# Kernel tuning notes

Measured on AMD Instinct MI355X. Metric: run time of the kernel, lower is better.

Reference implementation:

```python
import jax, jax.numpy as jnp
import numpy as np

B, L, DIM = 4, 2048, 512
H, D = 8, 64
SCALE = D ** -0.5
NEG = -10000.0


def setup_inputs() -> dict:
    key = jax.random.key(0)
    ks = jax.random.split(key, 5)
    std = 1.0 / np.sqrt(DIM)
    return {
        "x": jax.random.normal(ks[0], (B, L, DIM), dtype=jnp.float32),
        "wq": jax.random.normal(ks[1], (H * D, DIM), dtype=jnp.float32) * std,
        "wk": jax.random.normal(ks[2], (H * D, DIM), dtype=jnp.float32) * std,
        "wv": jax.random.normal(ks[3], (H * D, DIM), dtype=jnp.float32) * std,
        "wo": jax.random.normal(ks[4], (DIM, H * D), dtype=jnp.float32) * std,
    }


def reference(x, wq, wk, wv, wo):
    b, l, _ = x.shape
    # projections (torch Linear: y = x @ W.T), split heads -> [b,h,l,d]
    q = (x @ wq.T).reshape(b, l, H, D).transpose(0, 2, 1, 3)
    k = (x @ wk.T).reshape(b, l, H, D).transpose(0, 2, 1, 3)
    v = (x @ wv.T).reshape(b, l, H, D).transpose(0, 2, 1, 3)
    scores = jnp.einsum("bhld,bhsd->bhls", q, k) * SCALE
    scores = jnp.nan_to_num(scores, nan=0.0, posinf=10000.0, neginf=NEG)
    diag = jnp.eye(l, dtype=bool)[None, None]  # [1,1,l,l]
    scores = jnp.where(diag, NEG, scores)
    attn = jax.nn.softmax(scores, axis=-1)
    attn = jnp.where(diag, 0.0, attn)
    attn = jnp.nan_to_num(attn, nan=0.0, posinf=0.0, neginf=0.0)
    out = jnp.einsum("bhls,bhsd->bhld", attn, v)
    out = out.transpose(0, 2, 1, 3).reshape(b, l, H * D)
    return out @ wo.T
```

## Files before the change

### kernel.cpp

```cpp
#include <hip/hip_runtime.h>
#include <hip/hip_bf16.h>


#define Bsz 4
#define Lsz 2048
#define DIMsz 512
#define Hsz 8
#define Dsz 64

typedef _Float16 f16;
typedef __attribute__((ext_vector_type(8))) _Float16 f16x8;
typedef __attribute__((ext_vector_type(4))) _Float16 f16x4;
typedef __attribute__((ext_vector_type(4))) float f32x4;
typedef unsigned int u32;

#if __has_builtin(__builtin_amdgcn_exp2f)
#define EXP2(x) __builtin_amdgcn_exp2f(x)
#else
#define EXP2(x) __expf(0.6931471805599453f * (x))
#endif

__device__ __forceinline__ void gl2lds16(const void* g, void* l) {
    __builtin_amdgcn_global_load_lds(
        (const __attribute__((address_space(1))) u32*)g,
        (__attribute__((address_space(3))) u32*)l, 16, 0, 0);
}

__global__ __launch_bounds__(256) void pack_f16(
    const float* __restrict__ x, const float* __restrict__ wq,
    const float* __restrict__ wk, const float* __restrict__ wv,
    const float* __restrict__ wo,
    f16* __restrict__ xh, f16* __restrict__ w3h, f16* __restrict__ woh)
{
    const int seg = blockIdx.y;
    const float* s; f16* d; int n; float sc = 1.0f;
    switch (seg) {
        case 0: s = x;  d = xh;            n = 4194304; break;
        case 1: s = wq; d = w3h;           n = 262144; sc = 0.18033688011112042f; break;
        case 2: s = wk; d = w3h + 262144;  n = 262144; break;
        case 3: s = wv; d = w3h + 524288;  n = 262144; break;
        default: s = wo; d = woh;          n = 262144; break;
    }
    int i = (blockIdx.x * 256 + threadIdx.x) * 4;
    if (i >= n) return;
    float4 v = *(const float4*)(s + i);
    f16x4 o;
    o.x = (f16)(v.x * sc); o.y = (f16)(v.y * sc);
    o.z = (f16)(v.z * sc); o.w = (f16)(v.w * sc);
    *(f16x4*)(d + i) = o;
}

__global__ __launch_bounds__(256) void gemm_qkv_f16(
    const f16* __restrict__ A, const f16* __restrict__ B,
    f16* __restrict__ qh, f16* __restrict__ kh, f16* __restrict__ vth)
{
    __shared__ __align__(16) char smem[17408];
    f16* Ash = (f16*)smem;
    f16* Bsh = (f16*)(smem + 8192);

    const int tid = threadIdx.x;
    const int w = tid >> 6, lane = tid & 63;
    const int quad = lane >> 4, low = lane & 15;
    const int wm = w >> 1, wn = w & 1;
    const int m0 = blockIdx.y * 128, n0 = blockIdx.x * 128;

    f32x4 acc[4][4];
    #pragma unroll
    for (int i = 0; i < 4; i++)
        #pragma unroll
        for (int j = 0; j < 4; j++) acc[i][j] = (f32x4){0.f, 0.f, 0.f, 0.f};

    #pragma unroll 1
    for (int k0 = 0; k0 < DIMsz; k0 += 32) {
        __syncthreads();
        #pragma unroll
        for (int j = 0; j < 2; j++) {
            int t = j * 256 + tid;
            int r = t >> 2, g = t & 3;
            int gc = (g ^ ((r >> 1) & 3)) * 8;
            char* lb = (char*)Ash + (j * 256 + w * 64) * 16;
            gl2lds16(A + (size_t)(m0 + r) * DIMsz + k0 + gc, lb);
            char* lb2 = (char*)Bsh + (j * 256 + w * 64) * 16;
            gl2lds16(B + (size_t)(n0 + r) * DIMsz + k0 + gc, lb2);
        }
        __syncthreads();

        f16x8 af[4], bf[4];
        #pragma unroll
        for (int mt = 0; mt < 4; mt++) {
            int ar = wm * 64 + mt * 16 + low;
            af[mt] = *(const f16x8*)&Ash[ar * 32 + ((quad ^ ((ar >> 1) & 3)) << 3)];
        }
        #pragma unroll
        for (int nt = 0; nt < 4; nt++) {
            int br = wn * 64 + nt * 16 + low;
            bf[nt] = *(const f16x8*)&Bsh[br * 32 + ((quad ^ ((br >> 1) & 3)) << 3)];
        }
        #pragma unroll
        for (int mt = 0; mt < 4; mt++)
            #pragma unroll
            for (int nt = 0; nt < 4; nt++)
                acc[mt][nt] = __builtin_amdgcn_mfma_f32_16x16x32_f16(
                    af[mt], bf[nt], acc[mt][nt], 0, 0, 0);
    }

    const int proj = n0 >> 9;
    if (proj < 2) {
        f16* dst = (proj == 0) ? qh : kh;
        #pragma unroll
        for (int nt = 0; nt < 4; nt++) {
            int n = n0 + wn * 64 + nt * 16 + low;
            int c = n & 511, h = c >> 6, d = c & 63;
            #pragma unroll
            for (int mt = 0; mt < 4; mt++)
                #pragma unroll
                for (int r = 0; r < 4; r++) {
                    int m = m0 + wm * 64 + mt * 16 + quad * 4 + r;
                    int b_ = m >> 11, l = m & (Lsz - 1);
                    size_t bh = (size_t)(b_ * Hsz + h);
                    dst[(bh * Lsz + l) * Dsz + d] = (f16)acc[mt][nt][r];
                }
        }
    } else {
        const int hb = (n0 & 511) >> 6;
        f16* Tv = (f16*)smem;
        const int b_ = m0 >> 11, l0 = m0 & (Lsz - 1);
        #pragma unroll 1
        for (int hs = 0; hs < 2; hs++) {
            __syncthreads();
            if (wn == hs) {
                #pragma unroll
                for (int nt = 0; nt < 4; nt++) {
                    int d = nt * 16 + low;
                    #pragma unroll
                    for (int mt = 0; mt < 4; mt++)
                        #pragma unroll
                        for (int r = 0; r < 4; r++) {
                            int l = wm * 64 + mt * 16 + quad * 4 + r;
                            Tv[d * 136 + l] = (f16)acc[mt][nt][r];
                        }
                }
            }
            __syncthreads();
            int d = tid >> 2, seg = tid & 3;
            size_t bh = (size_t)(b_ * Hsz + hb + hs);
            f16* dstp = vth + (bh * 64 + d) * (size_t)Lsz + l0 + seg * 32;
            const f16* srcp = Tv + d * 136 + seg * 32;
            #pragma unroll
            for (int j = 0; j < 4; j++)
                *(f16x8*)(dstp + j * 8) = *(const f16x8*)(srcp + j * 8);
        }
    }
}

__global__ __launch_bounds__(256) void attn_mfma(
    const f16* __restrict__ q, const f16* __restrict__ k,
    const f16* __restrict__ vt, f16* __restrict__ ctx)
{
    __shared__ f16 Ks[64][72];
    __shared__ f16 Vs[64][72];
    __shared__ f16 Ps[4][16][72];

    const int tid = threadIdx.x;
    const int w = tid >> 6, lane = tid & 63;
    const int quad = lane >> 4, low = lane & 15;
    const int bh = blockIdx.y;
    const int bx64 = blockIdx.x * 64;
    const int q0 = bx64 + w * 16;
    const size_t kvb = (size_t)bh * Lsz;

    f16x8 qf[2];
    #pragma unroll
    for (int ks = 0; ks < 2; ks++)
        qf[ks] = *(const f16x8*)(q + (kvb + q0 + low) * Dsz + ks * 32 + quad * 8);

    f32x4 acc[4];
    float lsum[4];
    #pragma unroll
    for (int i = 0; i < 4; i++) { acc[i] = (f32x4){0.f, 0.f, 0.f, 0.f}; lsum[i] = 0.f; }

    #pragma unroll 1
    for (int s0 = 0; s0 < Lsz; s0 += 64) {
        __syncthreads();
        {
            const f16x8* kg = (const f16x8*)(k + (kvb + s0) * Dsz);
            const f16x8* vg = (const f16x8*)(vt + ((size_t)bh << 17) + s0);
            #pragma unroll
            for (int i = 0; i < 2; i++) {
                int idx = i * 256 + tid;
                int r = idx >> 3, g = idx & 7;
                *(f16x8*)&Ks[r][g * 8] = kg[idx];
                *(f16x8*)&Vs[r][g * 8] = vg[r * 256 + g];
            }
        }
        __syncthreads();

        f32x4 s[4];
        #pragma unroll
        for (int nt = 0; nt < 4; nt++) {
            f16x8 k0 = *(const f16x8*)&Ks[nt * 16 + low][quad * 8];
            f16x8 k1 = *(const f16x8*)&Ks[nt * 16 + low][32 + quad * 8];
            f32x4 t = {0.f, 0.f, 0.f, 0.f};
            t = __builtin_amdgcn_mfma_f32_16x16x32_f16(qf[0], k0, t, 0, 0, 0);
            t = __builtin_amdgcn_mfma_f32_16x16x32_f16(qf[1], k1, t, 0, 0, 0);
            s[nt] = t;
        }

        float pv[4][4];
        #pragma unroll
        for (int nt = 0; nt < 4; nt++)
            #pragma unroll
            for (int r = 0; r < 4; r++)
                pv[nt][r] = EXP2(s[nt][r]);
        if (s0 == bx64) {
            #pragma unroll
            for (int nt = 0; nt < 4; nt++)
                #pragma unroll
                for (int r = 0; r < 4; r++) {
                    bool dg = (nt == w) && (low == quad * 4 + r);
                    pv[nt][r] = dg ? 0.f : pv[nt][r];
                }
        }
        #pragma unroll
        for (int nt = 0; nt < 4; nt++)
            #pragma unroll
            for (int r = 0; r < 4; r++) {
                lsum[r] += pv[nt][r];
                Ps[w][quad * 4 + r][nt * 16 + low] = (f16)pv[nt][r];
            }

        f16x8 pf[2];
        #pragma unroll
        for (int ks = 0; ks < 2; ks++)
            pf[ks] = *(const f16x8*)&Ps[w][low][ks * 32 + quad * 8];
        #pragma unroll
        for (int dt = 0; dt < 4; dt++) {
            f16x8 v0 = *(const f16x8*)&Vs[dt * 16 + low][quad * 8];
            f16x8 v1 = *(const f16x8*)&Vs[dt * 16 + low][32 + quad * 8];
            f32x4 a = acc[dt];
            a = __builtin_amdgcn_mfma_f32_16x16x32_f16(pf[0], v0, a, 0, 0, 0);
            a = __builtin_amdgcn_mfma_f32_16x16x32_f16(pf[1], v1, a, 0, 0, 0);
            acc[dt] = a;
        }
    }

    #pragma unroll
    for (int r = 0; r < 4; r++) {
        #pragma unroll
        for (int off = 1; off < 16; off <<= 1)
            lsum[r] += __shfl_xor(lsum[r], off);
    }

    const int b = bh >> 3, h = bh & 7;
    #pragma unroll
    for (int r = 0; r < 4; r++) {
        int row = q0 + quad * 4 + r;
        float inv = 1.0f / lsum[r];
        #pragma unroll
        for (int dt = 0; dt < 4; dt++)
            ctx[((size_t)(b * Lsz + row)) * DIMsz + h * 64 + dt * 16 + low] =
                (f16)(acc[dt][r] * inv);
    }
}

__global__ __launch_bounds__(256) void gemm_out_f16(
    const f16* __restrict__ A, const f16* __restrict__ B,
    float* __restrict__ C)
{
    __shared__ f16 Ash[64 * 32];
    __shared__ f16 Bsh[64 * 32];
    const int tid = threadIdx.x;
    const int w = tid >> 6, lane = tid & 63;
    const int quad = lane >> 4, low = lane & 15;
    const int wm = w >> 1, wn = w & 1;
    const int m0 = blockIdx.y * 64, n0 = blockIdx.x * 64;

    f32x4 acc[2][2];
    #pragma unroll
    for (int i = 0; i < 2; i++)
        #pragma unroll
        for (int j = 0; j < 2; j++) acc[i][j] = (f32x4){0.f, 0.f, 0.f, 0.f};

    #pragma unroll 1
    for (int k0 = 0; k0 < DIMsz; k0 += 32) {
        __syncthreads();
        {
            int r = tid >> 2, g = tid & 3;
            int gc = (g ^ ((r >> 1) & 3)) * 8;
            gl2lds16(A + (size_t)(m0 + r) * DIMsz + k0 + gc, (char*)Ash + w * 64 * 16);
            gl2lds16(B + (size_t)(n0 + r) * DIMsz + k0 + gc, (char*)Bsh + w * 64 * 16);
        }
        __syncthreads();

        f16x8 af[2], bf[2];
        #pragma unroll
        for (int mt = 0; mt < 2; mt++) {
            int ar = wm * 32 + mt * 16 + low;
            af[mt] = *(const f16x8*)&Ash[ar * 32 + ((quad ^ ((ar >> 1) & 3)) << 3)];
        }
        #pragma unroll
        for (int nt = 0; nt < 2; nt++) {
            int br = wn * 32 + nt * 16 + low;
            bf[nt] = *(const f16x8*)&Bsh[br * 32 + ((quad ^ ((br >> 1) & 3)) << 3)];
        }
        #pragma unroll
        for (int mt = 0; mt < 2; mt++)
            #pragma unroll
            for (int nt = 0; nt < 2; nt++)
                acc[mt][nt] = __builtin_amdgcn_mfma_f32_16x16x32_f16(
                    af[mt], bf[nt], acc[mt][nt], 0, 0, 0);
    }

    #pragma unroll
    for (int mt = 0; mt < 2; mt++)
        #pragma unroll
        for (int r = 0; r < 4; r++) {
            int m = m0 + wm * 32 + mt * 16 + quad * 4 + r;
            #pragma unroll
            for (int nt = 0; nt < 2; nt++) {
                int n = n0 + wn * 32 + nt * 16 + low;
                C[(size_t)m * DIMsz + n] = acc[mt][nt][r];
            }
        }
}

extern "C" void kernel_launch(void* const* d_in, const int* in_sizes, int n_in,
                              void* d_out, int out_size, void* d_ws, size_t ws_size,
                              hipStream_t stream) {
    const float* x  = (const float*)d_in[0];
    const float* wq = (const float*)d_in[1];
    const float* wk = (const float*)d_in[2];
    const float* wv = (const float*)d_in[3];
    const float* wo = (const float*)d_in[4];
    float* out = (float*)d_out;

    const size_t NTOK = (size_t)Bsz * Lsz;
    const size_t XSZ  = NTOK * DIMsz;

    f16* xh   = (f16*)d_ws;
    f16* w3h  = xh + XSZ;
    f16* woh  = w3h + 3 * 262144;
    f16* qh   = woh + 262144;
    f16* kh   = qh + XSZ;
    f16* vth  = kh + XSZ;
    f16* ctxh = vth + XSZ;

    dim3 gp(4096, 5);
    pack_f16<<<gp, 256, 0, stream>>>(x, wq, wk, wv, wo, xh, w3h, woh);

    dim3 g1(1536 / 128, NTOK / 128);
    gemm_qkv_f16<<<g1, 256, 0, stream>>>(xh, w3h, qh, kh, vth);

    dim3 g2(Lsz / 64, Bsz * Hsz);
    attn_mfma<<<g2, 256, 0, stream>>>(qh, kh, vth, ctxh);

    dim3 g3(DIMsz / 64, NTOK / 64);
    gemm_out_f16<<<g3, 256, 0, stream>>>(ctxh, woh, out);
}
```

Before: 193.7 us.

## Transpose attention MFMA operands so P stays per-lane, pack probabilities, swap grid order

The QK^T and PV MFMAs now take their operands in swapped order, so each lane holds scores for one query row. The row sum becomes a single scalar reduced with two shuffles, and the output is written as vectorized f16x4 stores. Probabilities are packed two per u32 with cvt_pkrtz into a padded LDS buffer, which reduces LDS write count and conversion work. The grid is reordered so head index is fastest, which changes how blocks are scheduled and how K/V are reused in L2. Round-toward-zero conversion slightly changes numerics.

```diff
diff --git a/kernel.cpp b/kernel.cpp
--- a/kernel.cpp
+++ b/kernel.cpp
@@ -11,6 +11,7 @@
 typedef _Float16 f16;
 typedef __attribute__((ext_vector_type(8))) _Float16 f16x8;
 typedef __attribute__((ext_vector_type(4))) _Float16 f16x4;
+typedef __attribute__((ext_vector_type(2))) __fp16 fp16x2;
 typedef __attribute__((ext_vector_type(4))) float f32x4;
 typedef unsigned int u32;
 
@@ -19,6 +20,16 @@
 #else
 #define EXP2(x) __expf(0.6931471805599453f * (x))
 #endif
+
+__device__ __forceinline__ u32 pack2(float a, float b) {
+#if __has_builtin(__builtin_amdgcn_cvt_pkrtz)
+    fp16x2 h = __builtin_amdgcn_cvt_pkrtz(a, b);
+    return __builtin_bit_cast(u32, h);
+#else
+    fp16x2 h; h.x = (__fp16)a; h.y = (__fp16)b;
+    return __builtin_bit_cast(u32, h);
+#endif
+}
 
 __device__ __forceinline__ void gl2lds16(const void* g, void* l) {
     __builtin_amdgcn_global_load_lds(
@@ -159,14 +170,14 @@
 {
     __shared__ f16 Ks[64][72];
     __shared__ f16 Vs[64][72];
-    __shared__ f16 Ps[4][16][72];
+    __shared__ u32 Ppk[4][640];
 
     const int tid = threadIdx.x;
     const int w = tid >> 6, lane = tid & 63;
     const int quad = lane >> 4, low = lane & 15;
-    const int bh = blockIdx.y;
-    const int bx64 = blockIdx.x * 64;
-    const int q0 = bx64 + w * 16;
+    const int bh = blockIdx.x;
+    const int qb64 = blockIdx.y * 64;
+    const int q0 = qb64 + w * 16;
     const size_t kvb = (size_t)bh * Lsz;
 
     f16x8 qf[2];
@@ -175,9 +186,9 @@
         qf[ks] = *(const f16x8*)(q + (kvb + q0 + low) * Dsz + ks * 32 + quad * 8);
 
     f32x4 acc[4];
-    float lsum[4];
-    #pragma unroll
-    for (int i = 0; i < 4; i++) { acc[i] = (f32x4){0.f, 0.f, 0.f, 0.f}; lsum[i] = 0.f; }
+    float lsum = 0.f;
+    #pragma unroll
+    for (int i = 0; i < 4; i++) acc[i] = (f32x4){0.f, 0.f, 0.f, 0.f};
 
     #pragma unroll 1
     for (int s0 = 0; s0 < Lsz; s0 += 64) {
@@ -195,71 +206,63 @@
         }
         __syncthreads();
 
-        f32x4 s[4];
+        f32x4 st[4];
         #pragma unroll
         for (int nt = 0; nt < 4; nt++) {
             f16x8 k0 = *(const f16x8*)&Ks[nt * 16 + low][quad * 8];
             f16x8 k1 = *(const f16x8*)&Ks[nt * 16 + low][32 + quad * 8];
             f32x4 t = {0.f, 0.f, 0.f, 0.f};
-            t = __builtin_amdgcn_mfma_f32_16x16x32_f16(qf[0], k0, t, 0, 0, 0);
-            t = __builtin_amdgcn_mfma_f32_16x16x32_f16(qf[1], k1, t, 0, 0, 0);
-            s[nt] = t;
-        }
-
-        float pv[4][4];
-        #pragma unroll
-        for (int nt = 0; nt < 4; nt++)
-            #pragma unroll
-            for (int r = 0; r < 4; r++)
-                pv[nt][r] = EXP2(s[nt][r]);
-        if (s0 == bx64) {
-            #pragma unroll
-            for (int nt = 0; nt < 4; nt++)
-                #pragma unroll
-                for (int r = 0; r < 4; r++) {
-                    bool dg = (nt == w) && (low == quad * 4 + r);
-                    pv[nt][r] = dg ? 0.f : pv[nt][r];
-                }
-        }
-        #pragma unroll
-        for (int nt = 0; nt < 4; nt++)
-            #pragma unroll
-            for (int r = 0; r < 4; r++) {
-                lsum[r] += pv[nt][r];
-                Ps[w][quad * 4 + r][nt * 16 + low] = (f16)pv[nt][r];
+            t = __builtin_amdgcn_mfma_f32_16x16x32_f16(k0, qf[0], t, 0, 0, 0);
+            t = __builtin_amdgcn_mfma_f32_16x16x32_f16(k1, qf[1], t, 0, 0, 0);
+            st[nt] = t;
+        }
+
+        #pragma unroll
+        for (int nt = 0; nt < 4; nt++) {
+            float p0 = EXP2(st[nt][0]), p1 = EXP2(st[nt][1]);
+            float p2 = EXP2(st[nt][2]), p3 = EXP2(st[nt][3]);
+            if (s0 == qb64 && nt == w) {
+                p0 = (low == quad * 4 + 0) ? 0.f : p0;
+                p1 = (low == quad * 4 + 1) ? 0.f : p1;
+                p2 = (low == quad * 4 + 2) ? 0.f : p2;
+                p3 = (low == quad * 4 + 3) ? 0.f : p3;
             }
-
-        f16x8 pf[2];
-        #pragma unroll
-        for (int ks = 0; ks < 2; ks++)
-            pf[ks] = *(const f16x8*)&Ps[w][low][ks * 32 + quad * 8];
+            lsum += (p0 + p1) + (p2 + p3);
+            int sp = nt * 8 + quad * 2;
+            Ppk[w][sp * 20 + low]        = pack2(p0, p1);
+            Ppk[w][(sp + 1) * 20 + low]  = pack2(p2, p3);
+        }
+
+        union { u32 u[4]; f16x8 v; } pf0, pf1;
+        #pragma unroll
+        for (int jj = 0; jj < 4; jj++) {
+            pf0.u[jj] = Ppk[w][(quad * 4 + jj) * 20 + low];
+            pf1.u[jj] = Ppk[w][(16 + quad * 4 + jj) * 20 + low];
+        }
+
         #pragma unroll
         for (int dt = 0; dt < 4; dt++) {
             f16x8 v0 = *(const f16x8*)&Vs[dt * 16 + low][quad * 8];
             f16x8 v1 = *(const f16x8*)&Vs[dt * 16 + low][32 + quad * 8];
             f32x4 a = acc[dt];
-            a = __builtin_amdgcn_mfma_f32_16x16x32_f16(pf[0], v0, a, 0, 0, 0);
-            a = __builtin_amdgcn_mfma_f32_16x16x32_f16(pf[1], v1, a, 0, 0, 0);
+            a = __builtin_amdgcn_mfma_f32_16x16x32_f16(v0, pf0.v, a, 0, 0, 0);
+            a = __builtin_amdgcn_mfma_f32_16x16x32_f16(v1, pf1.v, a, 0, 0, 0);
             acc[dt] = a;
         }
     }
 
-    #pragma unroll
-    for (int r = 0; r < 4; r++) {
-        #pragma unroll
-        for (int off = 1; off < 16; off <<= 1)
-            lsum[r] += __shfl_xor(lsum[r], off);
-    }
+    lsum += __shfl_xor(lsum, 16);
+    lsum += __shfl_xor(lsum, 32);
+    const float inv = 1.0f / lsum;
 
     const int b = bh >> 3, h = bh & 7;
-    #pragma unroll
-    for (int r = 0; r < 4; r++) {
-        int row = q0 + quad * 4 + r;
-        float inv = 1.0f / lsum[r];
-        #pragma unroll
-        for (int dt = 0; dt < 4; dt++)
-            ctx[((size_t)(b * Lsz + row)) * DIMsz + h * 64 + dt * 16 + low] =
-                (f16)(acc[dt][r] * inv);
+    f16* op = ctx + ((size_t)(b * Lsz + q0 + low)) * DIMsz + h * 64 + quad * 4;
+    #pragma unroll
+    for (int dt = 0; dt < 4; dt++) {
+        f16x4 o;
+        o.x = (f16)(acc[dt][0] * inv); o.y = (f16)(acc[dt][1] * inv);
+        o.z = (f16)(acc[dt][2] * inv); o.w = (f16)(acc[dt][3] * inv);
+        *(f16x4*)(op + dt * 16) = o;
     }
 }
 
@@ -351,7 +354,7 @@
     dim3 g1(1536 / 128, NTOK / 128);
     gemm_qkv_f16<<<g1, 256, 0, stream>>>(xh, w3h, qh, kh, vth);
 
-    dim3 g2(Lsz / 64, Bsz * Hsz);
+    dim3 g2(Bsz * Hsz, Lsz / 64);
     attn_mfma<<<g2, 256, 0, stream>>>(qh, kh, vth, ctxh);
 
     dim3 g3(DIMsz / 64, NTOK / 64);
```

Measured after the change: 188.7 us. 1.03x faster.
